# Performance work log

Measured on AMD Instinct MI355X. Metric: run time of the kernel, lower is better.

Reference implementation:

```python
import jax, jax.numpy as jnp
import numpy as np


def setup_inputs() -> dict:
    key = jax.random.key(0)
    ks = jax.random.split(key, 6)
    B, S, H, F, E = 4, 2048, 1024, 4096, 8
    x = jax.random.normal(ks[0], (B, S, H), dtype=jnp.float32)
    Wr = jax.random.normal(ks[1], (H, E), dtype=jnp.float32) * (1.0 / np.sqrt(H))
    br = jnp.zeros((E,), dtype=jnp.float32)
    W1 = jax.random.normal(ks[2], (E, H, F), dtype=jnp.float32) * (1.0 / np.sqrt(H))
    b1 = jnp.zeros((E, F), dtype=jnp.float32)
    W2 = jax.random.normal(ks[3], (E, F, H), dtype=jnp.float32) * (1.0 / np.sqrt(F))
    b2 = jnp.zeros((E, H), dtype=jnp.float32)
    b_buf = jnp.zeros((E,), dtype=jnp.float32)  # load-balancing bias buffer, zero-init
    return {"x": x, "b_buf": b_buf, "Wr": Wr, "br": br,
            "W1": W1, "b1": b1, "W2": W2, "b2": b2, "k": 2}


def reference(x, b_buf, Wr, br, W1, b1, W2, b2, k):
    # Router
    scores = jnp.einsum('bsh,he->bse', x, Wr) + br          # [B,S,E]
    probs = jax.nn.softmax(scores, axis=-1)
    # load_balancing: expert selection uses biased scores (b_buf pre-update)
    _, expert_id = jax.lax.top_k(probs + b_buf, k)          # [B,S,k] int
    # combine weights use unbiased probs
    p, _ = jax.lax.top_k(probs, k)                          # [B,S,k]
    # Dense-dispatch reference: run every expert MLP on all tokens,
    # then select via one-hot mask (same math as gather/scatter dispatch).
    h1 = jnp.einsum('bsh,ehf->ebsf', x, W1) + b1[:, None, None, :]
    h1 = jax.nn.gelu(h1, approximate=False)                 # torch nn.GELU = exact
    out_e = jnp.einsum('ebsf,efh->ebsh', h1, W2) + b2[:, None, None, :]
    E = W1.shape[0]
    onehot = (expert_id[None, :, :, :] == jnp.arange(E)[:, None, None, None]).astype(x.dtype)  # [E,B,S,k]
    out_k = jnp.einsum('ebsk,ebsh->bskh', onehot, out_e)    # scatter-combine per slot
    w = p / jnp.sum(p, axis=-1, keepdims=True)              # normalize top-k probs
    return jnp.einsum('bsk,bskh->bsh', w, out_k)
```

## Files before the change

kernel.cpp:

```cpp
#include <hip/hip_runtime.h>
#include <stdint.h>

#define NTOK 8192
#define H_ 1024
#define F_ 4096
#define E_ 8
#define ROWS_CAP 17408
#define MBLK 136

using f32x4  = __attribute__((ext_vector_type(4))) float;
using short8 = __attribute__((ext_vector_type(8))) short;

typedef __attribute__((address_space(1))) const uint32_t gu32;
typedef __attribute__((address_space(3))) uint32_t lu32;

__device__ __forceinline__ void glds16(const void* g, void* l) {
  __builtin_amdgcn_global_load_lds((gu32*)g, (lu32*)l, 16, 0, 0);
}

__device__ __forceinline__ ushort f2bf(float f) {
  union { float f; uint32_t u; } v; v.f = f;
  uint32_t r = (v.u + 0x7FFFu + ((v.u >> 16) & 1u)) >> 16;
  return (ushort)r;
}

__global__ void k_init(int* cnt, int* cur, int* tok, float* wl) {
  int i = blockIdx.x * 256 + threadIdx.x;
  if (i < E_) { cnt[i] = 0; cur[i] = 0; }
  if (i < ROWS_CAP) { tok[i] = -1; wl[i] = 0.f; }
}

__global__ __launch_bounds__(256) void k_transcvt(const float* __restrict__ W,
                                                  ushort* __restrict__ WT,
                                                  int R, int C) {
  __shared__ float t[64][65];
  int e = blockIdx.z;
  int c0 = blockIdx.x * 64, r0 = blockIdx.y * 64;
  const float* Wp = W + (size_t)e * R * C;
  ushort* Tp = WT + (size_t)e * R * C;
  int tx = threadIdx.x & 15, ty = threadIdx.x >> 4;
#pragma unroll
  for (int i = 0; i < 4; i++) {
    int lr = ty + i * 16;
    const float4 v = *(const float4*)&Wp[(size_t)(r0 + lr) * C + c0 + tx * 4];
    t[lr][tx * 4 + 0] = v.x; t[lr][tx * 4 + 1] = v.y;
    t[lr][tx * 4 + 2] = v.z; t[lr][tx * 4 + 3] = v.w;
  }
  __syncthreads();
#pragma unroll
  for (int i = 0; i < 4; i++) {
    int lc = ty + i * 16;
    ushort4 o;
    o.x = f2bf(t[tx * 4 + 0][lc]);
    o.y = f2bf(t[tx * 4 + 1][lc]);
    o.z = f2bf(t[tx * 4 + 2][lc]);
    o.w = f2bf(t[tx * 4 + 3][lc]);
    *(ushort4*)&Tp[(size_t)(c0 + lc) * R + r0 + tx * 4] = o;
  }
}

__global__ __launch_bounds__(256) void k_router(const float* __restrict__ x,
                                                const float* __restrict__ Wr,
                                                const float* __restrict__ br,
                                                const float* __restrict__ bbuf,
                                                int* cnt, int* te, float* tw) {
  int wid = threadIdx.x >> 6, lane = threadIdx.x & 63;
  int t = blockIdx.x * 4 + wid;
  const float* xp = x + (size_t)t * H_;
  double acc[E_];
#pragma unroll
  for (int e = 0; e < E_; e++) acc[e] = 0.0;
  for (int j = lane; j < H_; j += 64) {
    float xv = xp[j];
    const float4 w0 = *(const float4*)&Wr[j * 8];
    const float4 w1 = *(const float4*)&Wr[j * 8 + 4];
    acc[0] += (double)xv * (double)w0.x;
    acc[1] += (double)xv * (double)w0.y;
    acc[2] += (double)xv * (double)w0.z;
    acc[3] += (double)xv * (double)w0.w;
    acc[4] += (double)xv * (double)w1.x;
    acc[5] += (double)xv * (double)w1.y;
    acc[6] += (double)xv * (double)w1.z;
    acc[7] += (double)xv * (double)w1.w;
  }
#pragma unroll
  for (int e = 0; e < E_; e++)
    for (int s = 32; s > 0; s >>= 1) acc[e] += __shfl_xor(acc[e], s);
  if (lane == 0) {
    double s[E_], m = -1e300;
    for (int e = 0; e < E_; e++) { s[e] = acc[e] + (double)br[e]; if (s[e] > m) m = s[e]; }
    double pe[E_], sum = 0.0;
    for (int e = 0; e < E_; e++) { pe[e] = exp(s[e] - m); sum += pe[e]; }
    double pr[E_], bb[E_];
    for (int e = 0; e < E_; e++) { pr[e] = pe[e] / sum; bb[e] = pr[e] + (double)bbuf[e]; }
    int e0 = 0;
    for (int e = 1; e < E_; e++) if (bb[e] > bb[e0]) e0 = e;
    int e1 = (e0 == 0) ? 1 : 0;
    for (int e = 0; e < E_; e++) if (e != e0 && bb[e] > bb[e1]) e1 = e;
    int a0 = 0;
    for (int e = 1; e < E_; e++) if (pr[e] > pr[a0]) a0 = e;
    int a1 = (a0 == 0) ? 1 : 0;
    for (int e = 0; e < E_; e++) if (e != a0 && pr[e] > pr[a1]) a1 = e;
    double iv = 1.0 / (pr[a0] + pr[a1]);
    te[t * 2] = e0; te[t * 2 + 1] = e1;
    tw[t * 2] = (float)(pr[a0] * iv); tw[t * 2 + 1] = (float)(pr[a1] * iv);
    atomicAdd(&cnt[e0], 1); atomicAdd(&cnt[e1], 1);
  }
}

__global__ void k_offsets(const int* cnt, int* off) {
  if (threadIdx.x == 0 && blockIdx.x == 0) {
    int o = 0; off[0] = 0;
    for (int e = 0; e < E_; e++) { o += ((cnt[e] + 127) >> 7) << 7; off[e + 1] = o; }
  }
}

__global__ void k_build(const int* __restrict__ te, const float* __restrict__ tw,
                        const int* __restrict__ off, int* cur, int* tok, float* wl) {
  int t = blockIdx.x * 256 + threadIdx.x;
  if (t >= NTOK) return;
#pragma unroll
  for (int s = 0; s < 2; s++) {
    int e = te[t * 2 + s];
    int slot = atomicAdd(&cur[e], 1);
    int pos = off[e] + slot;
    tok[pos] = t; wl[pos] = tw[t * 2 + s];
  }
}

__global__ __launch_bounds__(256) void k_gather(const float* __restrict__ x,
                                                const int* __restrict__ tok,
                                                ushort* __restrict__ Xg) {
  int row = blockIdx.x;
  int t = tok[row];
  if (t < 0) return;
  const float4* src = (const float4*)(x + (size_t)t * H_);
  ushort4* dst = (ushort4*)(Xg + (size_t)row * H_);
  int i = threadIdx.x;
  float4 v = src[i];
  ushort4 o; o.x = f2bf(v.x); o.y = f2bf(v.y); o.z = f2bf(v.z); o.w = f2bf(v.w);
  dst[i] = o;
}

__global__ void k_zero(float* out) {
  size_t i = (size_t)blockIdx.x * 256 + threadIdx.x;
  float4 z; z.x = 0.f; z.y = 0.f; z.z = 0.f; z.w = 0.f;
  ((float4*)out)[i] = z;
}

template <int MODE>
__global__ __launch_bounds__(256) void k_gemm(const ushort* __restrict__ A,
                                              const ushort* __restrict__ BT,
                                              const float* __restrict__ bias,
                                              ushort* __restrict__ Cbf,
                                              float* __restrict__ Out,
                                              const int* __restrict__ off,
                                              const int* __restrict__ tok,
                                              const float* __restrict__ wl,
                                              int K, int N, int NT) {
  int nwg = gridDim.x;
  int cpx = nwg >> 3;
  int bid = blockIdx.x;
  int lid = (bid & 7) * cpx + (bid >> 3);
  int gsz = NT << 3;
  int g = lid / gsz, r = lid % gsz;
  int n = r >> 3;
  int m = (g << 3) + (r & 7);
  int row0 = m * 128;
  int lastoff = off[E_];
  if (row0 >= lastoff) return;
  int e = 0;
  while (off[e + 1] <= row0) e++;
  int n0 = n * 128;
  const ushort* Bp = BT + (size_t)e * (size_t)N * (size_t)K;

  __shared__ __align__(16) ushort As[128 * 32];
  __shared__ __align__(16) ushort Bs[128 * 32];

  int tid = threadIdx.x, lane = tid & 63, wid = tid >> 6;
  int wr = wid >> 1, wc = wid & 1;

  f32x4 acc[4][4];
#pragma unroll
  for (int mm = 0; mm < 4; mm++)
#pragma unroll
    for (int nn = 0; nn < 4; nn++) acc[mm][nn] = (f32x4){0.f, 0.f, 0.f, 0.f};

  int srow = (wid << 4) + (lane >> 2);
  int skb  = (lane & 3) << 4;
  const char* aG0 = (const char*)(A  + (size_t)(row0 + srow) * K) + skb;
  const char* aG1 = (const char*)(A  + (size_t)(row0 + 64 + srow) * K) + skb;
  const char* bG0 = (const char*)(Bp + (size_t)(n0 + srow) * K) + skb;
  const char* bG1 = (const char*)(Bp + (size_t)(n0 + 64 + srow) * K) + skb;
  ushort* lA0 = As + (wid << 9);
  ushort* lA1 = lA0 + 2048;
  ushort* lB0 = Bs + (wid << 9);
  ushort* lB1 = lB0 + 2048;

  int fr = lane & 15, fq = lane >> 4;
  int aOff0 = ((wr << 6) + fr) * 32 + (fq << 3);
  int bOff0 = ((wc << 6) + fr) * 32 + (fq << 3);

  int nk = K >> 5;
  for (int kk = 0; kk < nk; kk++) {
    size_t kb = (size_t)kk << 6;
    __syncthreads();
    glds16(aG0 + kb, lA0);
    glds16(aG1 + kb, lA1);
    glds16(bG0 + kb, lB0);
    glds16(bG1 + kb, lB1);
    __syncthreads();
    short8 af[4], bfr[4];
#pragma unroll
    for (int mm = 0; mm < 4; mm++) af[mm] = *(const short8*)&As[aOff0 + mm * 16 * 32];
#pragma unroll
    for (int nn = 0; nn < 4; nn++) bfr[nn] = *(const short8*)&Bs[bOff0 + nn * 16 * 32];
#pragma unroll
    for (int mm = 0; mm < 4; mm++)
#pragma unroll
      for (int nn = 0; nn < 4; nn++)
        acc[mm][nn] = __builtin_amdgcn_mfma_f32_16x16x32_bf16(af[mm], bfr[nn], acc[mm][nn], 0, 0, 0);
  }

  const float* bp = bias + (size_t)e * N;
  if (MODE == 0) {
#pragma unroll
    for (int mm = 0; mm < 4; mm++)
#pragma unroll
      for (int nn = 0; nn < 4; nn++)
#pragma unroll
        for (int j = 0; j < 4; j++) {
          int rr = row0 + (wr << 6) + mm * 16 + (fq << 2) + j;
          int c = n0 + (wc << 6) + nn * 16 + fr;
          float v = acc[mm][nn][j] + bp[c];
          v = 0.5f * v * (1.0f + erff(v * 0.70710678118654752f));
          Cbf[(size_t)rr * (size_t)N + c] = f2bf(v);
        }
  } else {
#pragma unroll
    for (int mm = 0; mm < 4; mm++)
#pragma unroll
      for (int j = 0; j < 4; j++) {
        int rr = row0 + (wr << 6) + mm * 16 + (fq << 2) + j;
        int t = tok[rr];
        if (t < 0) continue;
        float w = wl[rr];
#pragma unroll
        for (int nn = 0; nn < 4; nn++) {
          int c = n0 + (wc << 6) + nn * 16 + fr;
          atomicAdd(&Out[(size_t)t * (size_t)N + c], w * (acc[mm][nn][j] + bp[c]));
        }
      }
  }
}

extern "C" void kernel_launch(void* const* d_in, const int* in_sizes, int n_in,
                              void* d_out, int out_size, void* d_ws, size_t ws_size,
                              hipStream_t stream) {
  (void)in_sizes; (void)n_in; (void)out_size; (void)ws_size;
  const float* x    = (const float*)d_in[0];
  const float* bbuf = (const float*)d_in[1];
  const float* Wr   = (const float*)d_in[2];
  const float* br   = (const float*)d_in[3];
  const float* W1   = (const float*)d_in[4];
  const float* b1   = (const float*)d_in[5];
  const float* W2   = (const float*)d_in[6];
  const float* b2   = (const float*)d_in[7];
  float* out = (float*)d_out;

  char* ws = (char*)d_ws;
  ushort* W1T = (ushort*)ws;
  ushort* W2T = (ushort*)(ws + 67108864);
  ushort* Xg  = (ushort*)(ws + 134217728);
  ushort* h1  = (ushort*)(ws + 169869312);
  char* meta  = ws + 312475648;
  int*   cnt = (int*)(meta);
  int*   off = (int*)(meta + 64);
  int*   cur = (int*)(meta + 128);
  int*   te  = (int*)(meta + 256);
  float* tw  = (float*)(meta + 256 + 65536);
  int*   tok = (int*)(meta + 256 + 131072);
  float* wl  = (float*)(meta + 256 + 131072 + 69632);

  k_init<<<ROWS_CAP / 256, 256, 0, stream>>>(cnt, cur, tok, wl);
  k_transcvt<<<dim3(F_ / 64, H_ / 64, E_), 256, 0, stream>>>(W1, W1T, H_, F_);
  k_transcvt<<<dim3(H_ / 64, F_ / 64, E_), 256, 0, stream>>>(W2, W2T, F_, H_);
  k_router<<<NTOK / 4, 256, 0, stream>>>(x, Wr, br, bbuf, cnt, te, tw);
  k_offsets<<<1, 64, 0, stream>>>(cnt, off);
  k_build<<<NTOK / 256, 256, 0, stream>>>(te, tw, off, cur, tok, wl);
  k_gather<<<ROWS_CAP, 256, 0, stream>>>(x, tok, Xg);
  k_zero<<<(NTOK * H_ / 4) / 256, 256, 0, stream>>>(out);
  k_gemm<0><<<32 * MBLK, 256, 0, stream>>>(Xg, W1T, b1, h1, nullptr, off, nullptr, nullptr, H_, F_, 32);
  k_gemm<1><<<8 * MBLK, 256, 0, stream>>>(h1, W2T, b2, nullptr, out, off, tok, wl, F_, H_, 8);
}
```

Measured before the change: 934.7 us.

## Double-buffer LDS tiles with BK=64, XOR swizzle, and prefetch overlap

Rewrites the grouped expert GEMM main loop to use two LDS buffers with a 64-wide K tile. The next tile is prefetched via global_load_lds while MFMAs run on the current one, with an explicit vmcnt wait instead of two full syncthreads per step. An XOR swizzle on the LDS column index reduces bank conflicts, and setprio raises wave priority during the MFMA sections. LDS use grows fourfold, which may reduce occupancy.

```diff
diff --git a/kernel.cpp b/kernel.cpp
--- a/kernel.cpp
+++ b/kernel.cpp
@@ -174,8 +174,8 @@
   int n0 = n * 128;
   const ushort* Bp = BT + (size_t)e * (size_t)N * (size_t)K;
 
-  __shared__ __align__(16) ushort As[128 * 32];
-  __shared__ __align__(16) ushort Bs[128 * 32];
+  __shared__ __align__(16) ushort As[2][128 * 64];
+  __shared__ __align__(16) ushort Bs[2][128 * 64];
 
   int tid = threadIdx.x, lane = tid & 63, wid = tid >> 6;
   int wr = wid >> 1, wc = wid & 1;
@@ -186,40 +186,62 @@
 #pragma unroll
     for (int nn = 0; nn < 4; nn++) acc[mm][nn] = (f32x4){0.f, 0.f, 0.f, 0.f};
 
-  int srow = (wid << 4) + (lane >> 2);
-  int skb  = (lane & 3) << 4;
-  const char* aG0 = (const char*)(A  + (size_t)(row0 + srow) * K) + skb;
-  const char* aG1 = (const char*)(A  + (size_t)(row0 + 64 + srow) * K) + skb;
-  const char* bG0 = (const char*)(Bp + (size_t)(n0 + srow) * K) + skb;
-  const char* bG1 = (const char*)(Bp + (size_t)(n0 + 64 + srow) * K) + skb;
-  ushort* lA0 = As + (wid << 9);
-  ushort* lA1 = lA0 + 2048;
-  ushort* lB0 = Bs + (wid << 9);
-  ushort* lB1 = lB0 + 2048;
+  int lr = lane >> 3;
+  int lc = lane & 7;
+  int csw = lc ^ lr;
+  const ushort* aSrc = A  + (size_t)(row0 + (wid << 5) + lr) * K + (csw << 3);
+  const ushort* bSrc = Bp + (size_t)(n0  + (wid << 5) + lr) * K + (csw << 3);
+  int ldsW = (wid << 11);
+  size_t jStep = (size_t)8 * K;
 
   int fr = lane & 15, fq = lane >> 4;
-  int aOff0 = ((wr << 6) + fr) * 32 + (fq << 3);
-  int bOff0 = ((wc << 6) + fr) * 32 + (fq << 3);
-
-  int nk = K >> 5;
+  int arow = (wr << 6) + fr;
+  int brow = (wc << 6) + fr;
+  int sw = fr & 7;
+
+  int nk = K >> 6;
+
+#pragma unroll
+  for (int j = 0; j < 4; j++) {
+    glds16(aSrc + j * jStep, &As[0][ldsW + j * 512]);
+    glds16(bSrc + j * jStep, &Bs[0][ldsW + j * 512]);
+  }
+
   for (int kk = 0; kk < nk; kk++) {
-    size_t kb = (size_t)kk << 6;
-    __syncthreads();
-    glds16(aG0 + kb, lA0);
-    glds16(aG1 + kb, lA1);
-    glds16(bG0 + kb, lB0);
-    glds16(bG1 + kb, lB1);
-    __syncthreads();
-    short8 af[4], bfr[4];
-#pragma unroll
-    for (int mm = 0; mm < 4; mm++) af[mm] = *(const short8*)&As[aOff0 + mm * 16 * 32];
-#pragma unroll
-    for (int nn = 0; nn < 4; nn++) bfr[nn] = *(const short8*)&Bs[bOff0 + nn * 16 * 32];
-#pragma unroll
-    for (int mm = 0; mm < 4; mm++)
+    int cur = kk & 1;
+    if (kk + 1 < nk) {
+      size_t ko = (size_t)(kk + 1) << 6;
+#pragma unroll
+      for (int j = 0; j < 4; j++) {
+        glds16(aSrc + j * jStep + ko, &As[cur ^ 1][ldsW + j * 512]);
+        glds16(bSrc + j * jStep + ko, &Bs[cur ^ 1][ldsW + j * 512]);
+      }
+      asm volatile("s_waitcnt vmcnt(8)" ::: "memory");
+    } else {
+      asm volatile("s_waitcnt vmcnt(0)" ::: "memory");
+    }
+    __builtin_amdgcn_s_barrier();
+    __builtin_amdgcn_sched_barrier(0);
+
+#pragma unroll
+    for (int ks = 0; ks < 2; ks++) {
+      short8 af[4], bfm[4];
+#pragma unroll
+      for (int mm = 0; mm < 4; mm++)
+        af[mm] = *(const short8*)&As[cur][(arow + mm * 16) * 64 + ((((ks << 2) + fq)) ^ sw) * 8];
 #pragma unroll
       for (int nn = 0; nn < 4; nn++)
-        acc[mm][nn] = __builtin_amdgcn_mfma_f32_16x16x32_bf16(af[mm], bfr[nn], acc[mm][nn], 0, 0, 0);
+        bfm[nn] = *(const short8*)&Bs[cur][(brow + nn * 16) * 64 + ((((ks << 2) + fq)) ^ sw) * 8];
+      __builtin_amdgcn_s_setprio(1);
+#pragma unroll
+      for (int mm = 0; mm < 4; mm++)
+#pragma unroll
+        for (int nn = 0; nn < 4; nn++)
+          acc[mm][nn] = __builtin_amdgcn_mfma_f32_16x16x32_bf16(af[mm], bfm[nn], acc[mm][nn], 0, 0, 0);
+      __builtin_amdgcn_s_setprio(0);
+    }
+    __builtin_amdgcn_sched_barrier(0);
+    __builtin_amdgcn_s_barrier();
   }
 
   const float* bp = bias + (size_t)e * N;
```

After: 984.5 us. 1.05x slower.

## Use 256x256 double-buffered GEMM tiles with compact row mapping and split-K

Applied to the files above, without the earlier changes.

The expert GEMMs move from 128x128 tiles with 256 threads and single-buffered LDS to 256x256 tiles with 512 threads. The new kernel uses 128KB of dynamic LDS, double-buffered async global-to-LDS loads, an XOR swizzle against bank conflicts, and setprio around the MFMA blocks. Gathered activations and h1 are now stored compactly, with no padded rows, through a virtual-to-compact row map. The second GEMM splits K into two halves that are combined by atomic adds. Exact erf GELU is replaced by the tanh approximation, which lowers epilogue cost but adds numerical deviation from the reference, which uses exact GELU.

```diff
diff --git a/kernel.cpp b/kernel.cpp
--- a/kernel.cpp
+++ b/kernel.cpp
@@ -5,8 +5,9 @@
 #define H_ 1024
 #define F_ 4096
 #define E_ 8
-#define ROWS_CAP 17408
-#define MBLK 136
+#define VCAP 18432
+#define VMBLK 72
+#define NCOMP 16384
 
 using f32x4  = __attribute__((ext_vector_type(4))) float;
 using short8 = __attribute__((ext_vector_type(8))) short;
@@ -24,10 +25,17 @@
   return (ushort)r;
 }
 
-__global__ void k_init(int* cnt, int* cur, int* tok, float* wl) {
+__device__ __forceinline__ float gelu_t(float x) {
+  float u = 0.7978845608028654f * (x + 0.044715f * x * x * x);
+  float e = exp2f(u * 2.885390081777927f);
+  float th = 1.0f - 2.0f / (1.0f + e);
+  return 0.5f * x * (1.0f + th);
+}
+
+__global__ void k_init(int* cnt, int* cur, int* tok, float* wl, int* v2c) {
   int i = blockIdx.x * 256 + threadIdx.x;
   if (i < E_) { cnt[i] = 0; cur[i] = 0; }
-  if (i < ROWS_CAP) { tok[i] = -1; wl[i] = 0.f; }
+  if (i < VCAP) { tok[i] = -1; wl[i] = 0.f; v2c[i] = -1; }
 }
 
 __global__ __launch_bounds__(256) void k_transcvt(const float* __restrict__ W,
@@ -108,32 +116,38 @@
   }
 }
 
-__global__ void k_offsets(const int* cnt, int* off) {
+__global__ void k_offsets(const int* cnt, int* off, int* coff) {
   if (threadIdx.x == 0 && blockIdx.x == 0) {
-    int o = 0; off[0] = 0;
-    for (int e = 0; e < E_; e++) { o += ((cnt[e] + 127) >> 7) << 7; off[e + 1] = o; }
+    int o = 0, c = 0;
+    for (int e = 0; e < E_; e++) {
+      off[e] = o; coff[e] = c;
+      o += ((cnt[e] + 255) >> 8) << 8;
+      c += cnt[e];
+    }
+    off[E_] = o; coff[E_] = c;
   }
 }
 
 __global__ void k_build(const int* __restrict__ te, const float* __restrict__ tw,
-                        const int* __restrict__ off, int* cur, int* tok, float* wl) {
+                        const int* __restrict__ off, const int* __restrict__ coff,
+                        int* cur, int* tok, float* wl, int* v2c, int* ctok) {
   int t = blockIdx.x * 256 + threadIdx.x;
   if (t >= NTOK) return;
 #pragma unroll
   for (int s = 0; s < 2; s++) {
     int e = te[t * 2 + s];
     int slot = atomicAdd(&cur[e], 1);
-    int pos = off[e] + slot;
-    tok[pos] = t; wl[pos] = tw[t * 2 + s];
+    int vp = off[e] + slot;
+    int cp = coff[e] + slot;
+    tok[vp] = t; wl[vp] = tw[t * 2 + s]; v2c[vp] = cp; ctok[cp] = t;
   }
 }
 
 __global__ __launch_bounds__(256) void k_gather(const float* __restrict__ x,
-                                                const int* __restrict__ tok,
+                                                const int* __restrict__ ctok,
                                                 ushort* __restrict__ Xg) {
   int row = blockIdx.x;
-  int t = tok[row];
-  if (t < 0) return;
+  int t = ctok[row];
   const float4* src = (const float4*)(x + (size_t)t * H_);
   ushort4* dst = (ushort4*)(Xg + (size_t)row * H_);
   int i = threadIdx.x;
@@ -149,108 +163,149 @@
 }
 
 template <int MODE>
-__global__ __launch_bounds__(256) void k_gemm(const ushort* __restrict__ A,
-                                              const ushort* __restrict__ BT,
-                                              const float* __restrict__ bias,
-                                              ushort* __restrict__ Cbf,
-                                              float* __restrict__ Out,
-                                              const int* __restrict__ off,
-                                              const int* __restrict__ tok,
-                                              const float* __restrict__ wl,
-                                              int K, int N, int NT) {
+__global__ __launch_bounds__(512, 2) void k_gemm(const ushort* __restrict__ A,
+                                                 const ushort* __restrict__ BT,
+                                                 const float* __restrict__ bias,
+                                                 ushort* __restrict__ h1,
+                                                 float* __restrict__ Out,
+                                                 const int* __restrict__ off,
+                                                 const int* __restrict__ v2c,
+                                                 const int* __restrict__ tok,
+                                                 const float* __restrict__ wl,
+                                                 int K, int N, int NTe) {
+  extern __shared__ char lds[];
   int nwg = gridDim.x;
   int cpx = nwg >> 3;
   int bid = blockIdx.x;
   int lid = (bid & 7) * cpx + (bid >> 3);
-  int gsz = NT << 3;
+  int gsz = NTe << 2;
   int g = lid / gsz, r = lid % gsz;
-  int n = r >> 3;
-  int m = (g << 3) + (r & 7);
-  int row0 = m * 128;
-  int lastoff = off[E_];
-  if (row0 >= lastoff) return;
+  int ne = r >> 2, m = (g << 2) + (r & 3);
+  int row0 = m << 8;
+  if (row0 >= off[E_]) return;
   int e = 0;
   while (off[e + 1] <= row0) e++;
-  int n0 = n * 128;
+  int n0, k0, nk;
+  if (MODE == 0) { n0 = ne << 8; k0 = 0; nk = K >> 6; }
+  else           { n0 = (ne >> 1) << 8; k0 = (ne & 1) * (K >> 1); nk = K >> 7; }
   const ushort* Bp = BT + (size_t)e * (size_t)N * (size_t)K;
 
-  __shared__ __align__(16) ushort As[128 * 32];
-  __shared__ __align__(16) ushort Bs[128 * 32];
-
-  int tid = threadIdx.x, lane = tid & 63, wid = tid >> 6;
-  int wr = wid >> 1, wc = wid & 1;
-
-  f32x4 acc[4][4];
-#pragma unroll
-  for (int mm = 0; mm < 4; mm++)
+  int tid = threadIdx.x, lane = tid & 63, w = tid >> 6;
+  int wr = w >> 2, wc = w & 3;
+
+  f32x4 acc[8][4];
+#pragma unroll
+  for (int mm = 0; mm < 8; mm++)
 #pragma unroll
     for (int nn = 0; nn < 4; nn++) acc[mm][nn] = (f32x4){0.f, 0.f, 0.f, 0.f};
 
-  int srow = (wid << 4) + (lane >> 2);
-  int skb  = (lane & 3) << 4;
-  const char* aG0 = (const char*)(A  + (size_t)(row0 + srow) * K) + skb;
-  const char* aG1 = (const char*)(A  + (size_t)(row0 + 64 + srow) * K) + skb;
-  const char* bG0 = (const char*)(Bp + (size_t)(n0 + srow) * K) + skb;
-  const char* bG1 = (const char*)(Bp + (size_t)(n0 + 64 + srow) * K) + skb;
-  ushort* lA0 = As + (wid << 9);
-  ushort* lA1 = lA0 + 2048;
-  ushort* lB0 = Bs + (wid << 9);
-  ushort* lB1 = lB0 + 2048;
+  int ur = lane >> 2;
+  int uc = lane & 3;
+  int gr = (ur & 3) ^ ((ur >> 2) & 3);
+  int sc = uc ^ gr;
+  int vr0 = row0 + (w << 4) + ur;
+  int cr0 = v2c[vr0];       if (cr0 < 0) cr0 = 0;
+  int cr1 = v2c[vr0 + 128]; if (cr1 < 0) cr1 = 0;
+  const char* aP0 = (const char*)(A + (size_t)cr0 * K) + k0 * 2 + sc * 16;
+  const char* aP1 = (const char*)(A + (size_t)cr1 * K) + k0 * 2 + sc * 16;
+  const char* bP0 = (const char*)(Bp + (size_t)(n0 + (w << 4) + ur) * K) + k0 * 2 + sc * 16;
+  const char* bP1 = (const char*)(Bp + (size_t)(n0 + 128 + (w << 4) + ur) * K) + k0 * 2 + sc * 16;
 
   int fr = lane & 15, fq = lane >> 4;
-  int aOff0 = ((wr << 6) + fr) * 32 + (fq << 3);
-  int bOff0 = ((wc << 6) + fr) * 32 + (fq << 3);
-
-  int nk = K >> 5;
-  for (int kk = 0; kk < nk; kk++) {
-    size_t kb = (size_t)kk << 6;
-    __syncthreads();
-    glds16(aG0 + kb, lA0);
-    glds16(aG1 + kb, lA1);
-    glds16(bG0 + kb, lB0);
-    glds16(bG1 + kb, lB1);
-    __syncthreads();
-    short8 af[4], bfr[4];
-#pragma unroll
-    for (int mm = 0; mm < 4; mm++) af[mm] = *(const short8*)&As[aOff0 + mm * 16 * 32];
-#pragma unroll
-    for (int nn = 0; nn < 4; nn++) bfr[nn] = *(const short8*)&Bs[bOff0 + nn * 16 * 32];
-#pragma unroll
-    for (int mm = 0; mm < 4; mm++)
-#pragma unroll
-      for (int nn = 0; nn < 4; nn++)
-        acc[mm][nn] = __builtin_amdgcn_mfma_f32_16x16x32_bf16(af[mm], bfr[nn], acc[mm][nn], 0, 0, 0);
-  }
+  int sg = (fr & 3) ^ ((fr >> 2) & 3);
+  int kchunk = (fq ^ sg) << 3;
+
+#define STAGE(tt, kss, bb) do {                                        \
+    size_t kb = (size_t)(tt) * 128 + (size_t)(kss) * 64;               \
+    char* db = lds + (bb) * 65536 + (kss) * 16384;                     \
+    glds16(aP0 + kb, db + (w << 10));                                  \
+    glds16(aP1 + kb, db + ((w + 8) << 10));                            \
+    glds16(bP0 + kb, db + 32768 + (w << 10));                          \
+    glds16(bP1 + kb, db + 32768 + ((w + 8) << 10));                    \
+  } while (0)
+
+#define COMPUTE(bb, kss) do {                                          \
+    const ushort* LA = (const ushort*)(lds + (bb) * 65536 + (kss) * 16384); \
+    const ushort* LB = LA + 16384;                                     \
+    short8 af[8], bfm[4];                                              \
+    _Pragma("unroll")                                                  \
+    for (int mm = 0; mm < 8; mm++)                                     \
+      af[mm] = *(const short8*)&LA[((wr << 7) + mm * 16 + fr) * 32 + kchunk]; \
+    _Pragma("unroll")                                                  \
+    for (int nn = 0; nn < 4; nn++)                                     \
+      bfm[nn] = *(const short8*)&LB[((wc << 6) + nn * 16 + fr) * 32 + kchunk]; \
+    __builtin_amdgcn_s_setprio(1);                                     \
+    _Pragma("unroll")                                                  \
+    for (int mm = 0; mm < 8; mm++)                                     \
+      _Pragma("unroll")                                                \
+      for (int nn = 0; nn < 4; nn++)                                   \
+        acc[mm][nn] = __builtin_amdgcn_mfma_f32_16x16x32_bf16(af[mm], bfm[nn], acc[mm][nn], 0, 0, 0); \
+    __builtin_amdgcn_s_setprio(0);                                     \
+  } while (0)
+
+  STAGE(0, 0, 0);
+  STAGE(0, 1, 0);
+  asm volatile("s_waitcnt vmcnt(4)" ::: "memory");
+  __builtin_amdgcn_s_barrier();
+  __builtin_amdgcn_sched_barrier(0);
+
+  for (int t = 0; t < nk; t++) {
+    int bb = t & 1;
+    if (t + 1 < nk) STAGE(t + 1, 0, bb ^ 1);
+    COMPUTE(bb, 0);
+    if (t + 1 < nk) asm volatile("s_waitcnt vmcnt(4)" ::: "memory");
+    else            asm volatile("s_waitcnt vmcnt(0)" ::: "memory");
+    __builtin_amdgcn_s_barrier();
+    __builtin_amdgcn_sched_barrier(0);
+    if (t + 1 < nk) {
+      STAGE(t + 1, 1, bb ^ 1);
+      COMPUTE(bb, 1);
+      asm volatile("s_waitcnt vmcnt(4)" ::: "memory");
+      __builtin_amdgcn_s_barrier();
+      __builtin_amdgcn_sched_barrier(0);
+    } else {
+      COMPUTE(bb, 1);
+    }
+  }
+#undef STAGE
+#undef COMPUTE
 
   const float* bp = bias + (size_t)e * N;
+  int cbase = n0 + (wc << 6);
   if (MODE == 0) {
 #pragma unroll
-    for (int mm = 0; mm < 4; mm++)
-#pragma unroll
-      for (int nn = 0; nn < 4; nn++)
-#pragma unroll
-        for (int j = 0; j < 4; j++) {
-          int rr = row0 + (wr << 6) + mm * 16 + (fq << 2) + j;
-          int c = n0 + (wc << 6) + nn * 16 + fr;
-          float v = acc[mm][nn][j] + bp[c];
-          v = 0.5f * v * (1.0f + erff(v * 0.70710678118654752f));
-          Cbf[(size_t)rr * (size_t)N + c] = f2bf(v);
-        }
-  } else {
-#pragma unroll
-    for (int mm = 0; mm < 4; mm++)
+    for (int mm = 0; mm < 8; mm++) {
 #pragma unroll
       for (int j = 0; j < 4; j++) {
-        int rr = row0 + (wr << 6) + mm * 16 + (fq << 2) + j;
-        int t = tok[rr];
-        if (t < 0) continue;
-        float w = wl[rr];
+        int vr = row0 + (wr << 7) + mm * 16 + (fq << 2) + j;
+        int cr = v2c[vr];
+        if (cr < 0) continue;
+        ushort* hp = h1 + (size_t)cr * N + cbase;
 #pragma unroll
         for (int nn = 0; nn < 4; nn++) {
-          int c = n0 + (wc << 6) + nn * 16 + fr;
-          atomicAdd(&Out[(size_t)t * (size_t)N + c], w * (acc[mm][nn][j] + bp[c]));
+          float v = acc[mm][nn][j] + bp[cbase + nn * 16 + fr];
+          hp[nn * 16 + fr] = f2bf(gelu_t(v));
         }
       }
+    }
+  } else {
+    bool addb = (k0 == 0);
+#pragma unroll
+    for (int mm = 0; mm < 8; mm++) {
+#pragma unroll
+      for (int j = 0; j < 4; j++) {
+        int vr = row0 + (wr << 7) + mm * 16 + (fq << 2) + j;
+        int t2 = tok[vr];
+        if (t2 < 0) continue;
+        float wgt = wl[vr];
+#pragma unroll
+        for (int nn = 0; nn < 4; nn++) {
+          int c = cbase + nn * 16 + fr;
+          float v = acc[mm][nn][j] + (addb ? bp[c] : 0.f);
+          atomicAdd(&Out[(size_t)t2 * (size_t)N + c], wgt * v);
+        }
+      }
+    }
   }
 }
 
@@ -272,24 +327,36 @@
   ushort* W1T = (ushort*)ws;
   ushort* W2T = (ushort*)(ws + 67108864);
   ushort* Xg  = (ushort*)(ws + 134217728);
-  ushort* h1  = (ushort*)(ws + 169869312);
-  char* meta  = ws + 312475648;
-  int*   cnt = (int*)(meta);
-  int*   off = (int*)(meta + 64);
-  int*   cur = (int*)(meta + 128);
-  int*   te  = (int*)(meta + 256);
-  float* tw  = (float*)(meta + 256 + 65536);
-  int*   tok = (int*)(meta + 256 + 131072);
-  float* wl  = (float*)(meta + 256 + 131072 + 69632);
-
-  k_init<<<ROWS_CAP / 256, 256, 0, stream>>>(cnt, cur, tok, wl);
+  ushort* h1  = (ushort*)(ws + 167772160);
+  char* meta  = ws + 301989888;
+  int*   cnt  = (int*)(meta);
+  int*   off  = (int*)(meta + 64);
+  int*   coff = (int*)(meta + 128);
+  int*   cur  = (int*)(meta + 192);
+  int*   te   = (int*)(meta + 256);
+  float* tw   = (float*)(meta + 65792);
+  int*   tok  = (int*)(meta + 131328);
+  float* wl   = (float*)(meta + 205056);
+  int*   v2c  = (int*)(meta + 278784);
+  int*   ctok = (int*)(meta + 352512);
+
+  hipFuncSetAttribute((const void*)&k_gemm<0>,
+                      hipFuncAttributeMaxDynamicSharedMemorySize, 131072);
+  hipFuncSetAttribute((const void*)&k_gemm<1>,
+                      hipFuncAttributeMaxDynamicSharedMemorySize, 131072);
+
+  k_init<<<VMBLK, 256, 0, stream>>>(cnt, cur, tok, wl, v2c);
   k_transcvt<<<dim3(F_ / 64, H_ / 64, E_), 256, 0, stream>>>(W1, W1T, H_, F_);
   k_transcvt<<<dim3(H_ / 64, F_ / 64, E_), 256, 0, stream>>>(W2, W2T, F_, H_);
   k_router<<<NTOK / 4, 256, 0, stream>>>(x, Wr, br, bbuf, cnt, te, tw);
-  k_offsets<<<1, 64, 0, stream>>>(cnt, off);
-  k_build<<<NTOK / 256, 256, 0, stream>>>(te, tw, off, cur, tok, wl);
-  k_gather<<<ROWS_CAP, 256, 0, stream>>>(x, tok, Xg);
+  k_offsets<<<1, 64, 0, stream>>>(cnt, off, coff);
+  k_build<<<NTOK / 256, 256, 0, stream>>>(te, tw, off, coff, cur, tok, wl, v2c, ctok);
+  k_gather<<<NCOMP, 256, 0, stream>>>(x, ctok, Xg);
   k_zero<<<(NTOK * H_ / 4) / 256, 256, 0, stream>>>(out);
-  k_gemm<0><<<32 * MBLK, 256, 0, stream>>>(Xg, W1T, b1, h1, nullptr, off, nullptr, nullptr, H_, F_, 32);
-  k_gemm<1><<<8 * MBLK, 256, 0, stream>>>(h1, W2T, b2, nullptr, out, off, tok, wl, F_, H_, 8);
-}
+  k_gemm<0><<<16 * VMBLK, 512, 131072, stream>>>(Xg, W1T, b1, h1, nullptr,
+                                                 off, v2c, nullptr, nullptr,
+                                                 H_, F_, 16);
+  k_gemm<1><<<8 * VMBLK, 512, 131072, stream>>>(h1, W2T, b2, nullptr, out,
+                                                off, v2c, tok, wl,
+                                                F_, H_, 8);
+}
```

Measured after the change: 2.275 ms. 2.43x slower.
